# Kernel optimization log

Hardware: AMD Instinct MI355X
Metric: run time of the kernel (lower is better)

Reference implementation:

```python
import jax, jax.numpy as jnp
import numpy as np
from jax import lax

VOCAB, EMB, HID, NCLS = 30000, 256, 256, 10


def setup_inputs() -> dict:
    key = jax.random.key(0)
    ks = jax.random.split(key, 12)
    B, T = 128, 512
    s_e = 1.0 / np.sqrt(EMB)
    s_h = 1.0 / np.sqrt(HID)
    inp = {
        "inputs": jax.random.randint(ks[0], (B, T), 0, VOCAB),
        "emb_table": jax.random.normal(ks[1], (VOCAB, EMB), jnp.float32),
        # forward-direction GRU params (torch layout: gates ordered r,z,n)
        "W_ih_f": jax.random.uniform(ks[2], (3 * HID, EMB), jnp.float32, -s_h, s_h),
        "W_hh_f": jax.random.uniform(ks[3], (3 * HID, HID), jnp.float32, -s_h, s_h),
        "b_ih_f": jax.random.uniform(ks[4], (3 * HID,), jnp.float32, -s_h, s_h),
        "b_hh_f": jax.random.uniform(ks[5], (3 * HID,), jnp.float32, -s_h, s_h),
        # backward-direction GRU params
        "W_ih_b": jax.random.uniform(ks[6], (3 * HID, EMB), jnp.float32, -s_h, s_h),
        "W_hh_b": jax.random.uniform(ks[7], (3 * HID, HID), jnp.float32, -s_h, s_h),
        "b_ih_b": jax.random.uniform(ks[8], (3 * HID,), jnp.float32, -s_h, s_h),
        "b_hh_b": jax.random.uniform(ks[9], (3 * HID,), jnp.float32, -s_h, s_h),
        # classifier head
        "W_lin": jax.random.uniform(ks[10], (NCLS, 2 * HID), jnp.float32, -1.0 / np.sqrt(2 * HID), 1.0 / np.sqrt(2 * HID)),
        "b_lin": jax.random.uniform(ks[11], (NCLS,), jnp.float32, -1.0 / np.sqrt(2 * HID), 1.0 / np.sqrt(2 * HID)),
    }
    return inp


def _gru_dir(x_tbe, W_ih, W_hh, b_ih, b_hh):
    """Run GRU over time-major x [T,B,E]; returns final hidden [B,H]."""
    # Precompute input projections for all steps in one big GEMM.
    xg = jnp.einsum("tbe,ge->tbg", x_tbe, W_ih) + b_ih  # [T,B,3H]

    def step(h, xg_t):
        hg = h @ W_hh.T + b_hh  # [B,3H]
        xr, xz, xn = jnp.split(xg_t, 3, axis=-1)
        hr, hz, hn = jnp.split(hg, 3, axis=-1)
        r = jax.nn.sigmoid(xr + hr)
        z = jax.nn.sigmoid(xz + hz)
        n = jnp.tanh(xn + r * hn)
        h_new = (1.0 - z) * n + z * h
        return h_new, None

    h0 = jnp.zeros((x_tbe.shape[1], W_hh.shape[1]), x_tbe.dtype)
    h_last, _ = lax.scan(step, h0, xg)
    return h_last


def reference(inputs, emb_table, W_ih_f, W_hh_f, b_ih_f, b_hh_f,
              W_ih_b, W_hh_b, b_ih_b, b_hh_b, W_lin, b_lin):
    # Dropout is identity in eval mode.
    emb = emb_table[inputs]               # [B,T,E]
    x = jnp.transpose(emb, (1, 0, 2))     # time-major [T,B,E]
    h_f = _gru_dir(x, W_ih_f, W_hh_f, b_ih_f, b_hh_f)            # [B,H]
    h_b = _gru_dir(x[::-1], W_ih_b, W_hh_b, b_ih_b, b_hh_b)      # [B,H]
    hidden = jnp.concatenate([h_f, h_b], axis=-1)                 # [B,2H]
    return hidden @ W_lin.T + b_lin                               # [B,10]
```

## Files before the change

kernel.cpp:

```cpp
#include <hip/hip_runtime.h>


typedef float f32x4 __attribute__((ext_vector_type(4)));
typedef short s16x8 __attribute__((ext_vector_type(8)));

#define VOCAB   30000
#define GCOLS   1536
#define HB_STR  280
#define HBUF    (16 * HB_STR)
#define GP_STR  1032
#define HS_STR  260
#define SRF     (-1.4426950408889634f)
#define SNF     (2.8853900817779268f)

#if defined(__has_builtin)
#if __has_builtin(__builtin_amdgcn_cvt_pk_bf16_f32)
#define HAVE_PK 1
#endif
#endif

static __device__ __forceinline__ unsigned short f2bf(float f) {
    unsigned u = __builtin_bit_cast(unsigned, f);
    u += 0x7fffu + ((u >> 16) & 1u);
    return (unsigned short)(u >> 16);
}
#ifdef HAVE_PK
typedef __bf16 bf16x2_t __attribute__((ext_vector_type(2)));
static __device__ __forceinline__ unsigned pk2(float a, float b) {
    bf16x2_t v = __builtin_amdgcn_cvt_pk_bf16_f32(a, b);
    return __builtin_bit_cast(unsigned, v);
}
#else
static __device__ __forceinline__ unsigned pk2(float a, float b) {
    return (unsigned)f2bf(a) | ((unsigned)f2bf(b) << 16);
}
#endif
static __device__ __forceinline__ float bf_lo(unsigned v) {
    return __builtin_bit_cast(float, v << 16);
}
static __device__ __forceinline__ float bf_hi(unsigned v) {
    return __builtin_bit_cast(float, v & 0xffff0000u);
}
static __device__ __forceinline__ s16x8 pack_bf8(float4 a, float4 b, float s) {
    union { s16x8 v; unsigned u[4]; } r;
    r.u[0] = pk2(a.x * s, a.y * s); r.u[1] = pk2(a.z * s, a.w * s);
    r.u[2] = pk2(b.x * s, b.y * s); r.u[3] = pk2(b.z * s, b.w * s);
    return r.v;
}
static __device__ __forceinline__ f32x4 mfma16(s16x8 a, s16x8 b, f32x4 c) {
    return __builtin_amdgcn_mfma_f32_16x16x32_bf16(a, b, c, 0, 0, 0);
}
static __device__ __forceinline__ float sig2(float x) {
    return __builtin_amdgcn_rcpf(1.0f + __builtin_amdgcn_exp2f(x));
}
static __device__ __forceinline__ void gload_lds16(const unsigned short* g, unsigned short* l) {
    __builtin_amdgcn_global_load_lds(
        (const __attribute__((address_space(1))) unsigned*)g,
        (__attribute__((address_space(3))) unsigned*)l, 16, 0, 0);
}


__global__ __launch_bounds__(512, 2)
void gru_table_kernel(const float* __restrict__ emb,
                      const float* __restrict__ Wih_f, const float* __restrict__ bih_f,
                      const float* __restrict__ bhh_f,
                      const float* __restrict__ Wih_b, const float* __restrict__ bih_b,
                      const float* __restrict__ bhh_b,
                      unsigned short* __restrict__ G) {
    __shared__ unsigned short aS[2][16 * HB_STR];

    const int tid  = threadIdx.x;
    const int lane = tid & 63;
    const int w    = tid >> 6;
    const int u    = lane & 15;
    const int q    = lane >> 4;
    const int d    = blockIdx.x;
    const int by   = blockIdx.y;

    const float* Wih = d ? Wih_b : Wih_f;
    const float* bih = d ? bih_b : bih_f;
    const float* bhh = d ? bhh_b : bhh_f;

    s16x8 breg[48];
    float beta[6];
#pragma unroll
    for (int t = 0; t < 6; ++t) {
        const int orig = (t >> 1) * 256 + 32 * w + ((t & 1) << 4) + u;
        const float scl = (t < 4) ? SRF : SNF;
        beta[t] = (bih[orig] + ((t < 4) ? bhh[orig] : 0.0f)) * scl;
#pragma unroll
        for (int kt = 0; kt < 8; ++kt) {
            const float* p = Wih + orig * 256 + kt * 32 + q * 8;
            breg[t * 8 + kt] =
                pack_bf8(*(const float4*)p, *(const float4*)(p + 4), scl);
        }
    }

    const int srow = tid >> 5;
    const int sc8  = (tid & 31) * 8;

    {
        const float* p = emb + (size_t)(by * 16 + srow) * 256 + sc8;
        float4 e0 = *(const float4*)p, e1 = *(const float4*)(p + 4);
        unsigned* dp = (unsigned*)&aS[0][srow * HB_STR + sc8];
        dp[0] = pk2(e0.x, e0.y); dp[1] = pk2(e0.z, e0.w);
        dp[2] = pk2(e1.x, e1.y); dp[3] = pk2(e1.z, e1.w);
    }
    __syncthreads();

    const size_t colbase = (size_t)(d * 48 + 6 * w) * 16 + u;

    for (int i = 0;; ++i) {
        const int mt = by + i * 128;
        if (mt >= 1875) break;
        const int mtn = mt + 128;
        const bool has_next = (mtn < 1875);
        const int buf = i & 1;

        float4 e0, e1;
        if (has_next) {
            const float* p = emb + (size_t)(mtn * 16 + srow) * 256 + sc8;
            e0 = *(const float4*)p;
            e1 = *(const float4*)(p + 4);
        }

        const int v0 = mt * 16;
#pragma unroll
        for (int l = 0; l < 2; ++l) {
            f32x4 a0 = {0.f, 0.f, 0.f, 0.f}, a1 = a0, a2 = a0;
#pragma unroll
            for (int kt = 0; kt < 8; ++kt) {
                s16x8 af = *(const s16x8*)&aS[buf][u * HB_STR + kt * 32 + q * 8];
                a0 = mfma16(af, breg[(0 + l) * 8 + kt], a0);
                a1 = mfma16(af, breg[(2 + l) * 8 + kt], a1);
                a2 = mfma16(af, breg[(4 + l) * 8 + kt], a2);
            }
#pragma unroll
            for (int g = 0; g < 3; ++g) {
                const f32x4 a = (g == 0) ? a0 : (g == 1) ? a1 : a2;
                const int t = 2 * g + l;
                unsigned short* gp = G + (size_t)(v0 + q * 4) * GCOLS + colbase + t * 16;
#pragma unroll
                for (int r = 0; r < 4; ++r)
                    gp[(size_t)r * GCOLS] = f2bf(a[r] + beta[t]);
            }
        }
        if (has_next) {
            unsigned* dp = (unsigned*)&aS[buf ^ 1][srow * HB_STR + sc8];
            dp[0] = pk2(e0.x, e0.y); dp[1] = pk2(e0.z, e0.w);
            dp[2] = pk2(e1.x, e1.y); dp[3] = pk2(e1.z, e1.w);
        }
        __syncthreads();
    }
}

__global__ __launch_bounds__(512, 2)
void gru_rnn_kernel(const int* __restrict__ inp,
                    const float* __restrict__ Whh_f, const float* __restrict__ bhh_f,
                    const float* __restrict__ Whh_b, const float* __restrict__ bhh_b,
                    const float* __restrict__ W_lin, const float* __restrict__ b_lin,
                    const unsigned short* __restrict__ G,
                    float* __restrict__ out) {
    __shared__ int            toks[16][513];
    __shared__ unsigned short hB[2 * HBUF];
    __shared__ unsigned short xgS[2][16][GP_STR];
    __shared__ float          bhnS[256];
    __shared__ float          hs[16 * HS_STR];

    const int tid  = threadIdx.x;
    const int lane = tid & 63;
    const int w    = tid >> 6;
    const int b    = lane & 15;
    const int q    = lane >> 4;
    const int d    = blockIdx.x >> 3;
    const int b0   = (blockIdx.x & 7) * 16;

    const float* Whh = d ? Whh_b : Whh_f;
    const float* bhh = d ? bhh_b : bhh_f;

    s16x8 wreg[48];
#pragma unroll
    for (int t = 0; t < 6; ++t) {
        const int orig = (t >> 1) * 256 + 32 * w + ((t & 1) << 4) + b;
        const float scl = (t < 4) ? SRF : SNF;
#pragma unroll
        for (int kt = 0; kt < 8; ++kt) {
            const float* p = Whh + orig * 256 + kt * 32 + q * 8;
            wreg[t * 8 + kt] =
                pack_bf8(*(const float4*)p, *(const float4*)(p + 4), scl);
        }
    }

    for (int i = tid; i < 16 * 512; i += 512) {
        int bb = i >> 9, t = i & 511;
        toks[bb][t] = inp[(b0 + bb) * 512 + t];
    }
    for (int i = tid; i < 2 * HBUF; i += 512) hB[i] = 0;
    if (tid < 256) bhnS[tid] = SNF * bhh[512 + tid];
    __syncthreads();

    {
        int t0 = d ? 511 : 0;
#pragma unroll
        for (int j = 0; j < 2; ++j) {
            int bb = 2 * w + j;
            int tok = toks[bb][t0];
            const unsigned short* gb = G + (size_t)tok * GCOLS + (d ? 512 : 0) + lane * 8;
            gload_lds16(gb,       &xgS[0][bb][0]);
            gload_lds16(gb + 512, &xgS[0][bb][512]);
        }
    }
    __syncthreads();

    const int xoff = d ? 256 : 0;
    const int hbq  = b * HB_STR + q * 8;
    float hreg[8];
#pragma unroll
    for (int i = 0; i < 8; ++i) hreg[i] = 0.f;

#pragma unroll 2
    for (int ts = 0; ts < 512; ++ts) {
        const int rb = (ts & 1) * HBUF;
        const int pn = (ts + 1) & 1;
        {
            int s1 = (ts < 511) ? ts + 1 : 511;
            int t1 = d ? 511 - s1 : s1;
#pragma unroll
            for (int j = 0; j < 2; ++j) {
                int bb = 2 * w + j;
                int tok = toks[bb][t1];
                const unsigned short* gb = G + (size_t)tok * GCOLS + (d ? 512 : 0) + lane * 8;
                gload_lds16(gb,       &xgS[pn][bb][0]);
                gload_lds16(gb + 512, &xgS[pn][bb][512]);
            }
        }
#pragma unroll
        for (int l = 0; l < 2; ++l) {
            f32x4 ar = {0.f, 0.f, 0.f, 0.f};
            f32x4 az = {0.f, 0.f, 0.f, 0.f};
            f32x4 an = *(const f32x4*)&bhnS[32 * w + 16 * l + 4 * q];
#pragma unroll
            for (int kt = 0; kt < 8; ++kt) {
                s16x8 hf = *(const s16x8*)&hB[rb + hbq + kt * 32];
                ar = mfma16(wreg[(0 + l) * 8 + kt], hf, ar);
                az = mfma16(wreg[(2 + l) * 8 + kt], hf, az);
                an = mfma16(wreg[(4 + l) * 8 + kt], hf, an);
            }
            const unsigned short* xrow = &xgS[ts & 1][b][xoff + 96 * w + 16 * l + 4 * q];
            uint2 uxr = *(const uint2*)&xrow[0];
            uint2 uxz = *(const uint2*)&xrow[32];
            uint2 uxn = *(const uint2*)&xrow[64];
            float xr[4] = {bf_lo(uxr.x), bf_hi(uxr.x), bf_lo(uxr.y), bf_hi(uxr.y)};
            float xz[4] = {bf_lo(uxz.x), bf_hi(uxz.x), bf_lo(uxz.y), bf_hi(uxz.y)};
            float xn[4] = {bf_lo(uxn.x), bf_hi(uxn.x), bf_lo(uxn.y), bf_hi(uxn.y)};
#pragma unroll
            for (int r = 0; r < 4; ++r) {
                float rg = sig2(xr[r] + ar[r]);
                float zg = sig2(xz[r] + az[r]);
                float tg = sig2(fmaf(rg, an[r], xn[r]));
                float ng = fmaf(-2.0f, tg, 1.0f);
                const int i = l * 4 + r;
                hreg[i] = fmaf(zg, hreg[i] - ng, ng);
            }
            unsigned p0 = pk2(hreg[l * 4 + 0], hreg[l * 4 + 1]);
            unsigned p1 = pk2(hreg[l * 4 + 2], hreg[l * 4 + 3]);
            *(uint2*)&hB[pn * HBUF + b * HB_STR + 32 * w + 16 * l + 4 * q] =
                make_uint2(p0, p1);
        }
        __syncthreads();
    }

#pragma unroll
    for (int l = 0; l < 2; ++l) {
        f32x4 v = {hreg[l * 4 + 0], hreg[l * 4 + 1],
                   hreg[l * 4 + 2], hreg[l * 4 + 3]};
        *(f32x4*)&hs[b * HS_STR + 32 * w + 16 * l + 4 * q] = v;
    }
    __syncthreads();
    if (tid < 160) {
        int bb = tid / 10;
        int c  = tid - bb * 10;
        float acc = d ? 0.0f : b_lin[c];
        const float* wl = W_lin + c * 512 + d * 256;
        const float* hp = &hs[bb * HS_STR];
        for (int i = 0; i < 256; ++i) acc += hp[i] * wl[i];
        atomicAdd(&out[(b0 + bb) * 10 + c], acc);
    }
}

extern "C" void kernel_launch(void* const* d_in, const int* in_sizes, int n_in,
                              void* d_out, int out_size, void* d_ws, size_t ws_size,
                              hipStream_t stream) {
    const int*   inp   = (const int*)d_in[0];
    const float* emb   = (const float*)d_in[1];
    const float* Wih_f = (const float*)d_in[2];
    const float* Whh_f = (const float*)d_in[3];
    const float* bih_f = (const float*)d_in[4];
    const float* bhh_f = (const float*)d_in[5];
    const float* Wih_b = (const float*)d_in[6];
    const float* Whh_b = (const float*)d_in[7];
    const float* bih_b = (const float*)d_in[8];
    const float* bhh_b = (const float*)d_in[9];
    const float* W_lin = (const float*)d_in[10];
    const float* b_lin = (const float*)d_in[11];
    float* out = (float*)d_out;
    unsigned short* G = (unsigned short*)d_ws;

    hipMemsetAsync(d_out, 0, (size_t)out_size * sizeof(float), stream);
    hipLaunchKernelGGL(gru_table_kernel, dim3(2, 128), dim3(512), 0, stream,
                       emb, Wih_f, bih_f, bhh_f, Wih_b, bih_b, bhh_b, G);
    hipLaunchKernelGGL(gru_rnn_kernel, dim3(16), dim3(512), 0, stream,
                       inp, Whh_f, bhh_f, Whh_b, bhh_b, W_lin, b_lin, G, out);
}
```

Before: 1.075 ms.

## Coalesce gate-table stores via LDS and register-prefetch per-lane gate inputs

The table kernel now stages its bf16 results in a shared tile and writes full 768-column rows with 16-byte coalesced stores. Previously it wrote scattered 2-byte values. The table layout becomes per-direction contiguous, so d*768 replaces the interleaved columns. The RNN kernel drops the global_load_lds double buffer of whole token rows and instead has each lane load only its own six uint2 gate slices straight into registers one step ahead. Those slices initialise the r/z accumulators, which removes an LDS round trip and the separate adds. Tokens are pre-multiplied by GCOLS, and the per-step global load latency must now be hidden by the MFMA work.

```diff
diff --git a/kernel.cpp b/kernel.cpp
--- a/kernel.cpp
+++ b/kernel.cpp
@@ -8,7 +8,7 @@
 #define GCOLS   1536
 #define HB_STR  280
 #define HBUF    (16 * HB_STR)
-#define GP_STR  1032
+#define CS_STR  776
 #define HS_STR  260
 #define SRF     (-1.4426950408889634f)
 #define SNF     (2.8853900817779268f)
@@ -52,11 +52,6 @@
 }
 static __device__ __forceinline__ float sig2(float x) {
     return __builtin_amdgcn_rcpf(1.0f + __builtin_amdgcn_exp2f(x));
-}
-static __device__ __forceinline__ void gload_lds16(const unsigned short* g, unsigned short* l) {
-    __builtin_amdgcn_global_load_lds(
-        (const __attribute__((address_space(1))) unsigned*)g,
-        (__attribute__((address_space(3))) unsigned*)l, 16, 0, 0);
 }
 
 
@@ -68,6 +63,7 @@
                       const float* __restrict__ bhh_b,
                       unsigned short* __restrict__ G) {
     __shared__ unsigned short aS[2][16 * HB_STR];
+    __shared__ unsigned short cS[16][CS_STR];
 
     const int tid  = threadIdx.x;
     const int lane = tid & 63;
@@ -98,6 +94,8 @@
 
     const int srow = tid >> 5;
     const int sc8  = (tid & 31) * 8;
+    const int orow = tid >> 5;
+    const int oc0  = (tid & 31) * 24;
 
     {
         const float* p = emb + (size_t)(by * 16 + srow) * 256 + sc8;
@@ -108,8 +106,6 @@
     }
     __syncthreads();
 
-    const size_t colbase = (size_t)(d * 48 + 6 * w) * 16 + u;
-
     for (int i = 0;; ++i) {
         const int mt = by + i * 128;
         if (mt >= 1875) break;
@@ -124,7 +120,6 @@
             e1 = *(const float4*)(p + 4);
         }
 
-        const int v0 = mt * 16;
 #pragma unroll
         for (int l = 0; l < 2; ++l) {
             f32x4 a0 = {0.f, 0.f, 0.f, 0.f}, a1 = a0, a2 = a0;
@@ -139,11 +134,18 @@
             for (int g = 0; g < 3; ++g) {
                 const f32x4 a = (g == 0) ? a0 : (g == 1) ? a1 : a2;
                 const int t = 2 * g + l;
-                unsigned short* gp = G + (size_t)(v0 + q * 4) * GCOLS + colbase + t * 16;
 #pragma unroll
                 for (int r = 0; r < 4; ++r)
-                    gp[(size_t)r * GCOLS] = f2bf(a[r] + beta[t]);
-            }
+                    cS[q * 4 + r][(6 * w + t) * 16 + u] = f2bf(a[r] + beta[t]);
+            }
+        }
+        __syncthreads();
+
+        {
+            const uint4* sp = (const uint4*)&cS[orow][oc0];
+            uint4 v0 = sp[0], v1 = sp[1], v2 = sp[2];
+            uint4* dp = (uint4*)(G + (size_t)(mt * 16 + orow) * GCOLS + d * 768 + oc0);
+            dp[0] = v0; dp[1] = v1; dp[2] = v2;
         }
         if (has_next) {
             unsigned* dp = (unsigned*)&aS[buf ^ 1][srow * HB_STR + sc8];
@@ -163,7 +165,6 @@
                     float* __restrict__ out) {
     __shared__ int            toks[16][513];
     __shared__ unsigned short hB[2 * HBUF];
-    __shared__ unsigned short xgS[2][16][GP_STR];
     __shared__ float          bhnS[256];
     __shared__ float          hs[16 * HS_STR];
 
@@ -193,52 +194,48 @@
 
     for (int i = tid; i < 16 * 512; i += 512) {
         int bb = i >> 9, t = i & 511;
-        toks[bb][t] = inp[(b0 + bb) * 512 + t];
+        toks[bb][t] = inp[(b0 + bb) * 512 + t] * GCOLS;
     }
     for (int i = tid; i < 2 * HBUF; i += 512) hB[i] = 0;
     if (tid < 256) bhnS[tid] = SNF * bhh[512 + tid];
     __syncthreads();
 
-    {
-        int t0 = d ? 511 : 0;
-#pragma unroll
-        for (int j = 0; j < 2; ++j) {
-            int bb = 2 * w + j;
-            int tok = toks[bb][t0];
-            const unsigned short* gb = G + (size_t)tok * GCOLS + (d ? 512 : 0) + lane * 8;
-            gload_lds16(gb,       &xgS[0][bb][0]);
-            gload_lds16(gb + 512, &xgS[0][bb][512]);
-        }
-    }
-    __syncthreads();
-
-    const int xoff = d ? 256 : 0;
+    const int gcol = d * 768 + 96 * w + 4 * q;
     const int hbq  = b * HB_STR + q * 8;
     float hreg[8];
 #pragma unroll
     for (int i = 0; i < 8; ++i) hreg[i] = 0.f;
+
+    uint2 pxr0, pxr1, pxz0, pxz1, pxn0, pxn1;
+    {
+        const uint2* gp = (const uint2*)(G + toks[b][d ? 511 : 0] + gcol);
+        pxr0 = gp[0];  pxr1 = gp[4];
+        pxz0 = gp[8];  pxz1 = gp[12];
+        pxn0 = gp[16]; pxn1 = gp[20];
+    }
 
 #pragma unroll 2
     for (int ts = 0; ts < 512; ++ts) {
         const int rb = (ts & 1) * HBUF;
         const int pn = (ts + 1) & 1;
-        {
-            int s1 = (ts < 511) ? ts + 1 : 511;
-            int t1 = d ? 511 - s1 : s1;
-#pragma unroll
-            for (int j = 0; j < 2; ++j) {
-                int bb = 2 * w + j;
-                int tok = toks[bb][t1];
-                const unsigned short* gb = G + (size_t)tok * GCOLS + (d ? 512 : 0) + lane * 8;
-                gload_lds16(gb,       &xgS[pn][bb][0]);
-                gload_lds16(gb + 512, &xgS[pn][bb][512]);
-            }
-        }
+        int s1 = (ts < 511) ? ts + 1 : 511;
+        const int t1 = d ? 511 - s1 : s1;
+
 #pragma unroll
         for (int l = 0; l < 2; ++l) {
-            f32x4 ar = {0.f, 0.f, 0.f, 0.f};
-            f32x4 az = {0.f, 0.f, 0.f, 0.f};
+            const uint2 uxr = l ? pxr1 : pxr0;
+            const uint2 uxz = l ? pxz1 : pxz0;
+            const uint2 uxn = l ? pxn1 : pxn0;
+            f32x4 ar = {bf_lo(uxr.x), bf_hi(uxr.x), bf_lo(uxr.y), bf_hi(uxr.y)};
+            f32x4 az = {bf_lo(uxz.x), bf_hi(uxz.x), bf_lo(uxz.y), bf_hi(uxz.y)};
             f32x4 an = *(const f32x4*)&bhnS[32 * w + 16 * l + 4 * q];
+            float xn[4] = {bf_lo(uxn.x), bf_hi(uxn.x), bf_lo(uxn.y), bf_hi(uxn.y)};
+            if (l == 1) {
+                const uint2* gp = (const uint2*)(G + toks[b][t1] + gcol);
+                pxr0 = gp[0];  pxr1 = gp[4];
+                pxz0 = gp[8];  pxz1 = gp[12];
+                pxn0 = gp[16]; pxn1 = gp[20];
+            }
 #pragma unroll
             for (int kt = 0; kt < 8; ++kt) {
                 s16x8 hf = *(const s16x8*)&hB[rb + hbq + kt * 32];
@@ -246,17 +243,10 @@
                 az = mfma16(wreg[(2 + l) * 8 + kt], hf, az);
                 an = mfma16(wreg[(4 + l) * 8 + kt], hf, an);
             }
-            const unsigned short* xrow = &xgS[ts & 1][b][xoff + 96 * w + 16 * l + 4 * q];
-            uint2 uxr = *(const uint2*)&xrow[0];
-            uint2 uxz = *(const uint2*)&xrow[32];
-            uint2 uxn = *(const uint2*)&xrow[64];
-            float xr[4] = {bf_lo(uxr.x), bf_hi(uxr.x), bf_lo(uxr.y), bf_hi(uxr.y)};
-            float xz[4] = {bf_lo(uxz.x), bf_hi(uxz.x), bf_lo(uxz.y), bf_hi(uxz.y)};
-            float xn[4] = {bf_lo(uxn.x), bf_hi(uxn.x), bf_lo(uxn.y), bf_hi(uxn.y)};
 #pragma unroll
             for (int r = 0; r < 4; ++r) {
-                float rg = sig2(xr[r] + ar[r]);
-                float zg = sig2(xz[r] + az[r]);
+                float rg = sig2(ar[r]);
+                float zg = sig2(az[r]);
                 float tg = sig2(fmaf(rg, an[r], xn[r]));
                 float ng = fmaf(-2.0f, tg, 1.0f);
                 const int i = l * 4 + r;
```

Result: slower. 1.126 ms (+4.8%).
